# Optimization experiments

Hardware: AMD Instinct MI355X
Metric: run time of the kernel (lower is better)

The kernel has to match this reference:

```python
import jax, jax.numpy as jnp
import numpy as np

N = 16        # state dim n
M = 8         # control dim m
T = 50        # time_steps
DT = 0.01     # delta_t
SQRT_DT = DT ** 0.5
GAMMA = 0.1
SIGMA = 0.2
TAU = 0.5
H = 10        # hidden width of subnets
BATCH = 32768


def _mlp(params, x):
    W1, b1, W2, b2, W3, b3 = params
    h = jnp.tanh(x @ W1 + b1)
    h = jnp.tanh(h @ W2 + b2)
    return h @ W3 + b3


def setup_inputs() -> dict:
    key = jax.random.key(0)
    ks = jax.random.split(key, 32)

    def dense(k, i, o):
        return (jax.random.normal(k, (i, o), jnp.float32) / np.float32(np.sqrt(i)))

    inp = {
        'dw': jax.random.normal(ks[0], (T, BATCH, 1), jnp.float32) * SQRT_DT,
        'X0': jax.random.uniform(ks[1], (BATCH, N), jnp.float32),
        'A': dense(ks[2], N, N),
        'Bmat': dense(ks[3], N, M),
        'Cmat': dense(ks[4], N, N),
        'Dmat': dense(ks[5], N, M),
        # phi: (n+1) -> 10 -> 10 -> m
        'phi_W1': dense(ks[6], N + 1, H), 'phi_b1': jnp.zeros((H,), jnp.float32),
        'phi_W2': dense(ks[7], H, H),     'phi_b2': jnp.zeros((H,), jnp.float32),
        'phi_W3': dense(ks[8], H, M),     'phi_b3': jnp.zeros((M,), jnp.float32),
        # Z: (n+1) -> 10 -> 10 -> n
        'Z_W1': dense(ks[9], N + 1, H),   'Z_b1': jnp.zeros((H,), jnp.float32),
        'Z_W2': dense(ks[10], H, H),      'Z_b2': jnp.zeros((H,), jnp.float32),
        'Z_W3': dense(ks[11], H, N),      'Z_b3': jnp.zeros((N,), jnp.float32),
        # Y0: n -> 10 -> 10 -> n
        'Y0_W1': dense(ks[12], N, H),     'Y0_b1': jnp.zeros((H,), jnp.float32),
        'Y0_W2': dense(ks[13], H, H),     'Y0_b2': jnp.zeros((H,), jnp.float32),
        'Y0_W3': dense(ks[14], H, N),     'Y0_b3': jnp.zeros((N,), jnp.float32),
    }
    return inp


def reference(dw, X0, A, Bmat, Cmat, Dmat,
              phi_W1, phi_b1, phi_W2, phi_b2, phi_W3, phi_b3,
              Z_W1, Z_b1, Z_W2, Z_b2, Z_W3, Z_b3,
              Y0_W1, Y0_b1, Y0_W2, Y0_b2, Y0_W3, Y0_b3):
    phi_p = (phi_W1, phi_b1, phi_W2, phi_b2, phi_W3, phi_b3)
    Z_p = (Z_W1, Z_b1, Z_W2, Z_b2, Z_W3, Z_b3)
    Y0_p = (Y0_W1, Y0_b1, Y0_W2, Y0_b2, Y0_W3, Y0_b3)

    B = X0.shape[0]
    Y = _mlp(Y0_p, X0)                              # [B, n]
    t_grid = jnp.arange(T, dtype=X0.dtype) * DT     # [T]
    w_trap = jnp.ones((T,), X0.dtype).at[1:-1].set(2.0)  # trapezoid weights

    def step(carry, xs):
        X, Yc, lc = carry
        dwi, t, w = xs                              # dwi: [B,1]
        state = jnp.concatenate(
            [jnp.broadcast_to(t, (B, 1)).astype(X.dtype), X], axis=1)  # [B, n+1]
        Zv = _mlp(Z_p, state)                       # [B, n]
        u = _mlp(phi_p, state)                      # [B, m] (project = identity)
        # b_mult(M, x) == x @ M.T
        drift_X = X @ A.T + u @ Bmat.T + GAMMA      # [B, n]
        diffusion_X = X @ Cmat.T + u @ Dmat.T + SIGMA
        drift_Y = -(Yc @ A + Zv @ Cmat + X)         # f_x(X,u) = X
        # stop_recording branch: gradient of dH / pre_phi
        dH = Yc @ Bmat + Zv @ Dmat + u              # f_u(X,u) = u -> [B, m]
        pre_phi = jax.lax.stop_gradient(u - TAU * dH)
        Xn = X + drift_X * DT + dwi * diffusion_X
        Yn = Yc + drift_Y * DT + dwi * Zv
        lc = lc + 0.5 * DT * w * jnp.sum(jnp.square(u - pre_phi), axis=1)
        return (Xn, Yn, lc), None

    init = (X0, Y, jnp.zeros((B,), X0.dtype))
    (X, Y, loss_control), _ = jax.lax.scan(step, init, (dw, t_grid, w_trap))
    loss_bsde = jnp.sum(jnp.square(Y - X), axis=1)  # g_x(X) = X
    return jnp.stack([jnp.mean(loss_bsde), jnp.mean(loss_control)])
```

## Files before the change

kernel.cpp:

```cpp
#include <hip/hip_runtime.h>

namespace {

typedef float v4f __attribute__((ext_vector_type(4)));
typedef _Float16 half8 __attribute__((ext_vector_type(8)));
typedef unsigned int uint32;

constexpr int   kB     = 32768;
constexpr int   kT     = 50;
constexpr float kDT    = 0.01f;
constexpr float kGamma = 0.1f;
constexpr float kSigma = 0.2f;
constexpr float kTau   = 0.5f;

constexpr int kWsDwords = 13 * 256;

__device__ __forceinline__ float ftanh(float x) {
  float e = exp2f(x * 2.8853900817779268f);
  return 1.0f - 2.0f * __builtin_amdgcn_rcpf(e + 1.0f);
}

__device__ __forceinline__ uint32 pk2(float a, float b) {
  union { _Float16 h[2]; uint32 u; } z;
  z.h[0] = (_Float16)a; z.h[1] = (_Float16)b;
  return z.u;
}

__device__ __forceinline__ v4f tanh4(v4f a) {
  v4f r;
  r[0] = ftanh(a[0]); r[1] = ftanh(a[1]);
  r[2] = ftanh(a[2]); r[3] = ftanh(a[3]);
  return r;
}

#define WAVE_FENCE() asm volatile("" ::: "memory")

__global__ __launch_bounds__(256) void prep_kernel(
    const float* __restrict__ A,   const float* __restrict__ Bm,
    const float* __restrict__ Cm,  const float* __restrict__ Dm,
    const float* __restrict__ pW1, const float* __restrict__ pb1,
    const float* __restrict__ pW2, const float* __restrict__ pb2,
    const float* __restrict__ pW3, const float* __restrict__ pb3,
    const float* __restrict__ zW1, const float* __restrict__ zb1,
    const float* __restrict__ zW2, const float* __restrict__ zb2,
    const float* __restrict__ zW3, const float* __restrict__ zb3,
    const float* __restrict__ yW1, const float* __restrict__ yb1,
    const float* __restrict__ yW2, const float* __restrict__ yb2,
    const float* __restrict__ yW3, const float* __restrict__ yb3,
    uint32* __restrict__ ws, float* __restrict__ out)
{
  const int tid = threadIdx.x;
  if (tid < 2) out[tid] = 0.0f;

  auto wval = [&](int p, int m, int k) -> float {
    switch (p) {
      case 0:
        if (m >= 10) return 0.f;
        if (k == 1) return yb1[m];
        if (k >= 2 && k < 18) return yW1[(k - 2) * 10 + m];
        return 0.f;
      case 1:
        if (m >= 10) return 0.f;
        if (k < 10) return yW2[k * 10 + m];
        if (k == 10) return yb2[m];
        return 0.f;
      case 2:
        if (k < 10) return yW3[k * 16 + m];
        if (k == 10) return yb3[m];
        return 0.f;
      case 3:
        if (m >= 10) return 0.f;
        if (k == 0) return zW1[m];
        if (k == 1) return zb1[m];
        if (k < 18) return zW1[(k - 1) * 10 + m];
        return 0.f;
      case 4:
        if (m >= 10) return 0.f;
        if (k == 0) return pW1[m];
        if (k == 1) return pb1[m];
        if (k < 18) return pW1[(k - 1) * 10 + m];
        return 0.f;
      case 5:
        if (m >= 10) return 0.f;
        if (k < 10) return zW2[k * 10 + m];
        if (k == 10) return zb2[m];
        return 0.f;
      case 6:
        if (m >= 10) return 0.f;
        if (k < 10) return pW2[k * 10 + m];
        if (k == 10) return pb2[m];
        return 0.f;
      case 7:
        if (k < 10) return zW3[k * 16 + m];
        if (k == 10) return zb3[m];
        return 0.f;
      case 8:
        if (m >= 8) return 0.f;
        if (k < 10) return pW3[k * 8 + m];
        if (k == 10) return pb3[m];
        return 0.f;
      case 9:
        if (k < 16) return A[m * 16 + k];
        if (k < 24) return Bm[m * 8 + (k - 16)];
        if (k == 24) return kGamma;
        return 0.f;
      case 10:
        if (k < 16) return Cm[m * 16 + k];
        if (k < 24) return Dm[m * 8 + (k - 16)];
        if (k == 24) return kSigma;
        return 0.f;
      case 11:
        if (k < 16) return A[k * 16 + m];
        return Cm[(k - 16) * 16 + m];
      case 12:
        if (m >= 8) return 0.f;
        if (k < 16) return Bm[k * 8 + m];
        return Dm[(k - 16) * 8 + m];
    }
    return 0.f;
  };

  for (int idx = tid; idx < kWsDwords; idx += 256) {
    int p = idx >> 8, r = idx & 255;
    int lane = r >> 2, dwi = r & 3;
    int m = lane & 15, q = lane >> 4;
    int k0 = 8 * q + 2 * dwi;
    ws[idx] = pk2(wval(p, m, k0), wval(p, m, k0 + 1));
  }
}

__global__ __launch_bounds__(64)
__attribute__((amdgpu_waves_per_eu(2, 2)))
void bsde_kernel(const float* __restrict__ dw, const float* __restrict__ X0,
                 const uint32* __restrict__ wsu, float* __restrict__ out)
{
  __shared__ __align__(16) uint32 S[7][16][20];
  constexpr int B1 = 0, HZ = 1, HP = 2, GZ = 3, GP = 4, XU = 5, YZ = 6;

  const int lane = threadIdx.x;
  const int col  = lane & 15;
  const int quad = lane >> 4;
  const int e    = blockIdx.x * 16 + col;

  half8 af[13];
#pragma unroll
  for (int p = 0; p < 13; ++p) {
    union { uint4 u; half8 h; } z;
    z.u = *(const uint4*)(wsu + p * 256 + lane * 4);
    af[p] = z.h;
  }

  auto readB = [&](int b) -> half8 {
    union { uint4 u; half8 h; } z;
    z.u = *(const uint4*)&S[b][col][4 * quad];
    return z.h;
  };
  auto writeH = [&](int b, v4f t) {
    if (quad < 2) {
      uint2 w = {pk2(t[0], t[1]), pk2(t[2], t[3])};
      *(uint2*)&S[b][col][2 * quad] = w;
    } else if (quad == 2) {
      uint2 w = {pk2(t[0], t[1]), pk2(1.f, 0.f)};
      *(uint2*)&S[b][col][4] = w;
    }
  };

  for (int i = lane; i < 7 * 16 * 20; i += 64) (&S[0][0][0])[i] = 0u;
  WAVE_FENCE();

  v4f x4 = *(const v4f*)&X0[e * 16 + 4 * quad];
  {
    uint32 p01 = pk2(x4[0], x4[1]), p23 = pk2(x4[2], x4[3]);
    S[B1][col][1 + 2 * quad] = p01;
    S[B1][col][2 + 2 * quad] = p23;
    uint2 w = {p01, p23};
    *(uint2*)&S[XU][col][2 * quad] = w;
    if (lane < 16) {
      S[B1][col][0]  = pk2(0.f, 1.f);
      S[XU][col][12] = pk2(1.f, 0.f);
    }
  }
  WAVE_FENCE();

  const v4f zero4 = {0.f, 0.f, 0.f, 0.f};

  v4f y4;
  {
    v4f d = __builtin_amdgcn_mfma_f32_16x16x32_f16(af[0], readB(B1), zero4, 0, 0, 0);
    writeH(HZ, tanh4(d));
    WAVE_FENCE();
    d = __builtin_amdgcn_mfma_f32_16x16x32_f16(af[1], readB(HZ), zero4, 0, 0, 0);
    writeH(GZ, tanh4(d));
    WAVE_FENCE();
    y4 = __builtin_amdgcn_mfma_f32_16x16x32_f16(af[2], readB(GZ), zero4, 0, 0, 0);
    uint2 w = {pk2(y4[0], y4[1]), pk2(y4[2], y4[3])};
    *(uint2*)&S[YZ][col][2 * quad] = w;
  }
  WAVE_FENCE();

  float lcp = 0.0f;
  float dwv = dw[e];

#pragma unroll 1
  for (int t = 0; t < kT; ++t) {
    float dwn = (t < kT - 1) ? dw[(t + 1) * kB + e] : 0.0f;
    const float tv = (float)t * kDT;
    const float wt = (t == 0 || t == kT - 1) ? 1.0f : 2.0f;

    if (lane < 16) S[B1][col][0] = pk2(tv, 1.f);
    WAVE_FENCE();

    half8 bs = readB(B1);
    v4f hz = __builtin_amdgcn_mfma_f32_16x16x32_f16(af[3], bs, zero4, 0, 0, 0);
    v4f hp = __builtin_amdgcn_mfma_f32_16x16x32_f16(af[4], bs, zero4, 0, 0, 0);
    writeH(HZ, tanh4(hz));
    writeH(HP, tanh4(hp));
    WAVE_FENCE();

    v4f gz = __builtin_amdgcn_mfma_f32_16x16x32_f16(af[5], readB(HZ), zero4, 0, 0, 0);
    v4f gp = __builtin_amdgcn_mfma_f32_16x16x32_f16(af[6], readB(HP), zero4, 0, 0, 0);
    writeH(GZ, tanh4(gz));
    writeH(GP, tanh4(gp));
    WAVE_FENCE();

    v4f zv = __builtin_amdgcn_mfma_f32_16x16x32_f16(af[7], readB(GZ), zero4, 0, 0, 0);
    v4f uu = __builtin_amdgcn_mfma_f32_16x16x32_f16(af[8], readB(GP), zero4, 0, 0, 0);
    {
      uint2 wz = {pk2(zv[0], zv[1]), pk2(zv[2], zv[3])};
      *(uint2*)&S[YZ][col][8 + 2 * quad] = wz;
      if (quad < 2) {
        uint2 wu = {pk2(uu[0], uu[1]), pk2(uu[2], uu[3])};
        *(uint2*)&S[XU][col][8 + 2 * quad] = wu;
      }
    }
    WAVE_FENCE();

    half8 bxu = readB(XU);
    half8 byz = readB(YZ);
    v4f dx = __builtin_amdgcn_mfma_f32_16x16x32_f16(af[9],  bxu, zero4, 0, 0, 0);
    v4f fx = __builtin_amdgcn_mfma_f32_16x16x32_f16(af[10], bxu, zero4, 0, 0, 0);
    v4f dy = __builtin_amdgcn_mfma_f32_16x16x32_f16(af[11], byz, zero4, 0, 0, 0);
    v4f dh = __builtin_amdgcn_mfma_f32_16x16x32_f16(af[12], byz, zero4, 0, 0, 0);

    float ss = 0.0f;
    v4f Xn, Yn;
#pragma unroll
    for (int r = 0; r < 4; ++r) {
      Xn[r] = x4[r] + kDT * dx[r] + dwv * fx[r];
      Yn[r] = y4[r] - kDT * (dy[r] + x4[r]) + dwv * zv[r];
      float d = dh[r] + uu[r];
      ss += d * d;
    }
    lcp += (0.5f * kDT * kTau * kTau) * wt * ss;
    x4 = Xn; y4 = Yn;

    {
      uint32 p01 = pk2(x4[0], x4[1]), p23 = pk2(x4[2], x4[3]);
      S[B1][col][1 + 2 * quad] = p01;
      S[B1][col][2 + 2 * quad] = p23;
      uint2 wx = {p01, p23};
      *(uint2*)&S[XU][col][2 * quad] = wx;
      uint2 wy = {pk2(y4[0], y4[1]), pk2(y4[2], y4[3])};
      *(uint2*)&S[YZ][col][2 * quad] = wy;
    }
    dwv = dwn;
    WAVE_FENCE();
  }

  float bp = 0.0f;
#pragma unroll
  for (int r = 0; r < 4; ++r) { float d = y4[r] - x4[r]; bp += d * d; }

#pragma unroll
  for (int s = 32; s > 0; s >>= 1) {
    bp  += __shfl_down(bp,  s, 64);
    lcp += __shfl_down(lcp, s, 64);
  }
  if (lane == 0) {
    atomicAdd(&out[0], bp  * (1.0f / (float)kB));
    atomicAdd(&out[1], lcp * (1.0f / (float)kB));
  }
}

}

extern "C" void kernel_launch(void* const* d_in, const int* in_sizes, int n_in,
                              void* d_out, int out_size, void* d_ws, size_t ws_size,
                              hipStream_t stream) {
  (void)in_sizes; (void)n_in; (void)ws_size; (void)out_size;

  const float* dw  = (const float*)d_in[0];
  const float* X0  = (const float*)d_in[1];
  const float* A   = (const float*)d_in[2];
  const float* Bm  = (const float*)d_in[3];
  const float* Cm  = (const float*)d_in[4];
  const float* Dm  = (const float*)d_in[5];
  const float* pW1 = (const float*)d_in[6];
  const float* pb1 = (const float*)d_in[7];
  const float* pW2 = (const float*)d_in[8];
  const float* pb2 = (const float*)d_in[9];
  const float* pW3 = (const float*)d_in[10];
  const float* pb3 = (const float*)d_in[11];
  const float* zW1 = (const float*)d_in[12];
  const float* zb1 = (const float*)d_in[13];
  const float* zW2 = (const float*)d_in[14];
  const float* zb2 = (const float*)d_in[15];
  const float* zW3 = (const float*)d_in[16];
  const float* zb3 = (const float*)d_in[17];
  const float* yW1 = (const float*)d_in[18];
  const float* yb1 = (const float*)d_in[19];
  const float* yW2 = (const float*)d_in[20];
  const float* yb2 = (const float*)d_in[21];
  const float* yW3 = (const float*)d_in[22];
  const float* yb3 = (const float*)d_in[23];
  float* out = (float*)d_out;
  unsigned int* ws = (unsigned int*)d_ws;

  prep_kernel<<<1, 256, 0, stream>>>(
      A, Bm, Cm, Dm,
      pW1, pb1, pW2, pb2, pW3, pb3,
      zW1, zb1, zW2, zb2, zW3, zb3,
      yW1, yb1, yW2, yb2, yW3, yb3, ws, out);

  bsde_kernel<<<kB / 16, 64, 0, stream>>>(dw, X0, ws, out);
}
```

Measured before the change: 218.9 us.

## Replace LDS staging of MFMA operands with cross-lane shuffles

Removes the shared-memory scratch buffers used to turn MFMA output fragments into B-operand fragments, and builds each operand in registers with __shfl. The first-layer weight packing is reordered so that the state vector occupies K slots 0-15 and time and bias sit at slots 16-17. The aim is to cut LDS write/read round trips and the wait latency on the serial per-step dependency chain. In exchange it adds many ds_bpermute shuffles and select instructions per step, which also go through the LDS hardware.

Result: no change. 216.8 us (-0.9%).

```diff
diff --git a/kernel.cpp b/kernel.cpp
--- a/kernel.cpp
+++ b/kernel.cpp
@@ -33,7 +33,7 @@
   return r;
 }
 
-#define WAVE_FENCE() asm volatile("" ::: "memory")
+union U8 { uint32 u[4]; half8 h; };
 
 __global__ __launch_bounds__(256) void prep_kernel(
     const float* __restrict__ A,   const float* __restrict__ Bm,
@@ -56,8 +56,8 @@
     switch (p) {
       case 0:
         if (m >= 10) return 0.f;
-        if (k == 1) return yb1[m];
-        if (k >= 2 && k < 18) return yW1[(k - 2) * 10 + m];
+        if (k < 16) return yW1[k * 10 + m];
+        if (k == 17) return yb1[m];
         return 0.f;
       case 1:
         if (m >= 10) return 0.f;
@@ -70,15 +70,15 @@
         return 0.f;
       case 3:
         if (m >= 10) return 0.f;
-        if (k == 0) return zW1[m];
-        if (k == 1) return zb1[m];
-        if (k < 18) return zW1[(k - 1) * 10 + m];
+        if (k < 16) return zW1[(k + 1) * 10 + m];
+        if (k == 16) return zW1[m];
+        if (k == 17) return zb1[m];
         return 0.f;
       case 4:
         if (m >= 10) return 0.f;
-        if (k == 0) return pW1[m];
-        if (k == 1) return pb1[m];
-        if (k < 18) return pW1[(k - 1) * 10 + m];
+        if (k < 16) return pW1[(k + 1) * 10 + m];
+        if (k == 16) return pW1[m];
+        if (k == 17) return pb1[m];
         return 0.f;
       case 5:
         if (m >= 10) return 0.f;
@@ -134,9 +134,6 @@
 void bsde_kernel(const float* __restrict__ dw, const float* __restrict__ X0,
                  const uint32* __restrict__ wsu, float* __restrict__ out)
 {
-  __shared__ __align__(16) uint32 S[7][16][20];
-  constexpr int B1 = 0, HZ = 1, HP = 2, GZ = 3, GP = 4, XU = 5, YZ = 6;
-
   const int lane = threadIdx.x;
   const int col  = lane & 15;
   const int quad = lane >> 4;
@@ -150,53 +147,47 @@
     af[p] = z.h;
   }
 
-  auto readB = [&](int b) -> half8 {
-    union { uint4 u; half8 h; } z;
-    z.u = *(const uint4*)&S[b][col][4 * quad];
-    return z.h;
+  const int srcA = col + ((quad & 1) << 5);
+  const int srcH = col + ((quad == 1) ? 32 : 0);
+  const uint32 pkONE = pk2(1.f, 0.f);
+  const v4f zero4 = {0.f, 0.f, 0.f, 0.f};
+
+  auto shf = [](uint32 v, int s) -> uint32 {
+    return (uint32)__shfl((int)v, s, 64);
   };
-  auto writeH = [&](int b, v4f t) {
-    if (quad < 2) {
-      uint2 w = {pk2(t[0], t[1]), pk2(t[2], t[3])};
-      *(uint2*)&S[b][col][2 * quad] = w;
-    } else if (quad == 2) {
-      uint2 w = {pk2(t[0], t[1]), pk2(1.f, 0.f)};
-      *(uint2*)&S[b][col][4] = w;
-    }
+
+  auto buildH = [&](v4f th) -> half8 {
+    uint32 p0 = pk2(th[0], th[1]), p1 = pk2(th[2], th[3]);
+    uint32 d0 = shf(p0, srcH);
+    uint32 d1 = shf(p1, srcH);
+    uint32 d2 = shf(p0, col + 16);
+    uint32 d3 = shf(p1, col + 16);
+    U8 f;
+    f.u[0] = (quad < 2)  ? d0 : 0u;
+    f.u[1] = (quad == 0) ? d1 : ((quad == 1) ? pkONE : 0u);
+    f.u[2] = (quad == 0) ? d2 : 0u;
+    f.u[3] = (quad == 0) ? d3 : 0u;
+    return f.h;
   };
 
-  for (int i = lane; i < 7 * 16 * 20; i += 64) (&S[0][0][0])[i] = 0u;
-  WAVE_FENCE();
-
   v4f x4 = *(const v4f*)&X0[e * 16 + 4 * quad];
-  {
-    uint32 p01 = pk2(x4[0], x4[1]), p23 = pk2(x4[2], x4[3]);
-    S[B1][col][1 + 2 * quad] = p01;
-    S[B1][col][2 + 2 * quad] = p23;
-    uint2 w = {p01, p23};
-    *(uint2*)&S[XU][col][2 * quad] = w;
-    if (lane < 16) {
-      S[B1][col][0]  = pk2(0.f, 1.f);
-      S[XU][col][12] = pk2(1.f, 0.f);
-    }
-  }
-  WAVE_FENCE();
-
-  const v4f zero4 = {0.f, 0.f, 0.f, 0.f};
-
   v4f y4;
   {
-    v4f d = __builtin_amdgcn_mfma_f32_16x16x32_f16(af[0], readB(B1), zero4, 0, 0, 0);
-    writeH(HZ, tanh4(d));
-    WAVE_FENCE();
-    d = __builtin_amdgcn_mfma_f32_16x16x32_f16(af[1], readB(HZ), zero4, 0, 0, 0);
-    writeH(GZ, tanh4(d));
-    WAVE_FENCE();
-    y4 = __builtin_amdgcn_mfma_f32_16x16x32_f16(af[2], readB(GZ), zero4, 0, 0, 0);
-    uint2 w = {pk2(y4[0], y4[1]), pk2(y4[2], y4[3])};
-    *(uint2*)&S[YZ][col][2 * quad] = w;
-  }
-  WAVE_FENCE();
+    uint32 xp0 = pk2(x4[0], x4[1]), xp1 = pk2(x4[2], x4[3]);
+    uint32 XD0 = shf(xp0, srcA),      XD1 = shf(xp1, srcA);
+    uint32 XD2 = shf(xp0, srcA + 16), XD3 = shf(xp1, srcA + 16);
+    uint32 pkT = pk2(0.f, 1.f);
+    U8 b1;
+    b1.u[0] = (quad < 2) ? XD0 : ((quad == 2) ? pkT : 0u);
+    b1.u[1] = (quad < 2) ? XD1 : 0u;
+    b1.u[2] = (quad < 2) ? XD2 : 0u;
+    b1.u[3] = (quad < 2) ? XD3 : 0u;
+    v4f h = __builtin_amdgcn_mfma_f32_16x16x32_f16(af[0], b1.h, zero4, 0, 0, 0);
+    half8 hf = buildH(tanh4(h));
+    v4f g = __builtin_amdgcn_mfma_f32_16x16x32_f16(af[1], hf, zero4, 0, 0, 0);
+    half8 gf = buildH(tanh4(g));
+    y4 = __builtin_amdgcn_mfma_f32_16x16x32_f16(af[2], gf, zero4, 0, 0, 0);
+  }
 
   float lcp = 0.0f;
   float dwv = dw[e];
@@ -207,40 +198,54 @@
     const float tv = (float)t * kDT;
     const float wt = (t == 0 || t == kT - 1) ? 1.0f : 2.0f;
 
-    if (lane < 16) S[B1][col][0] = pk2(tv, 1.f);
-    WAVE_FENCE();
-
-    half8 bs = readB(B1);
-    v4f hz = __builtin_amdgcn_mfma_f32_16x16x32_f16(af[3], bs, zero4, 0, 0, 0);
-    v4f hp = __builtin_amdgcn_mfma_f32_16x16x32_f16(af[4], bs, zero4, 0, 0, 0);
-    writeH(HZ, tanh4(hz));
-    writeH(HP, tanh4(hp));
-    WAVE_FENCE();
-
-    v4f gz = __builtin_amdgcn_mfma_f32_16x16x32_f16(af[5], readB(HZ), zero4, 0, 0, 0);
-    v4f gp = __builtin_amdgcn_mfma_f32_16x16x32_f16(af[6], readB(HP), zero4, 0, 0, 0);
-    writeH(GZ, tanh4(gz));
-    writeH(GP, tanh4(gp));
-    WAVE_FENCE();
-
-    v4f zv = __builtin_amdgcn_mfma_f32_16x16x32_f16(af[7], readB(GZ), zero4, 0, 0, 0);
-    v4f uu = __builtin_amdgcn_mfma_f32_16x16x32_f16(af[8], readB(GP), zero4, 0, 0, 0);
-    {
-      uint2 wz = {pk2(zv[0], zv[1]), pk2(zv[2], zv[3])};
-      *(uint2*)&S[YZ][col][8 + 2 * quad] = wz;
-      if (quad < 2) {
-        uint2 wu = {pk2(uu[0], uu[1]), pk2(uu[2], uu[3])};
-        *(uint2*)&S[XU][col][8 + 2 * quad] = wu;
-      }
-    }
-    WAVE_FENCE();
-
-    half8 bxu = readB(XU);
-    half8 byz = readB(YZ);
-    v4f dx = __builtin_amdgcn_mfma_f32_16x16x32_f16(af[9],  bxu, zero4, 0, 0, 0);
-    v4f fx = __builtin_amdgcn_mfma_f32_16x16x32_f16(af[10], bxu, zero4, 0, 0, 0);
-    v4f dy = __builtin_amdgcn_mfma_f32_16x16x32_f16(af[11], byz, zero4, 0, 0, 0);
-    v4f dh = __builtin_amdgcn_mfma_f32_16x16x32_f16(af[12], byz, zero4, 0, 0, 0);
+    uint32 xp0 = pk2(x4[0], x4[1]), xp1 = pk2(x4[2], x4[3]);
+    uint32 yp0 = pk2(y4[0], y4[1]), yp1 = pk2(y4[2], y4[3]);
+    uint32 XD0 = shf(xp0, srcA),      XD1 = shf(xp1, srcA);
+    uint32 XD2 = shf(xp0, srcA + 16), XD3 = shf(xp1, srcA + 16);
+    uint32 YD0 = shf(yp0, srcA),      YD1 = shf(yp1, srcA);
+    uint32 YD2 = shf(yp0, srcA + 16), YD3 = shf(yp1, srcA + 16);
+
+    uint32 pkT = pk2(tv, 1.f);
+    U8 b1;
+    b1.u[0] = (quad < 2) ? XD0 : ((quad == 2) ? pkT : 0u);
+    b1.u[1] = (quad < 2) ? XD1 : 0u;
+    b1.u[2] = (quad < 2) ? XD2 : 0u;
+    b1.u[3] = (quad < 2) ? XD3 : 0u;
+
+    v4f hz = __builtin_amdgcn_mfma_f32_16x16x32_f16(af[3], b1.h, zero4, 0, 0, 0);
+    v4f hp = __builtin_amdgcn_mfma_f32_16x16x32_f16(af[4], b1.h, zero4, 0, 0, 0);
+    half8 hzf = buildH(tanh4(hz));
+    half8 hpf = buildH(tanh4(hp));
+
+    v4f gz = __builtin_amdgcn_mfma_f32_16x16x32_f16(af[5], hzf, zero4, 0, 0, 0);
+    v4f gp = __builtin_amdgcn_mfma_f32_16x16x32_f16(af[6], hpf, zero4, 0, 0, 0);
+    half8 gzf = buildH(tanh4(gz));
+    half8 gpf = buildH(tanh4(gp));
+
+    v4f zv = __builtin_amdgcn_mfma_f32_16x16x32_f16(af[7], gzf, zero4, 0, 0, 0);
+    v4f uu = __builtin_amdgcn_mfma_f32_16x16x32_f16(af[8], gpf, zero4, 0, 0, 0);
+
+    uint32 up0 = pk2(uu[0], uu[1]), up1 = pk2(uu[2], uu[3]);
+    uint32 zp0 = pk2(zv[0], zv[1]), zp1 = pk2(zv[2], zv[3]);
+    uint32 UD0 = shf(up0, col),      UD1 = shf(up1, col);
+    uint32 UD2 = shf(up0, col + 16), UD3 = shf(up1, col + 16);
+    uint32 ZD0 = shf(zp0, srcA),      ZD1 = shf(zp1, srcA);
+    uint32 ZD2 = shf(zp0, srcA + 16), ZD3 = shf(zp1, srcA + 16);
+
+    U8 xu, yz;
+    xu.u[0] = (quad < 2) ? XD0 : ((quad == 2) ? UD0 : pkONE);
+    xu.u[1] = (quad < 2) ? XD1 : ((quad == 2) ? UD1 : 0u);
+    xu.u[2] = (quad < 2) ? XD2 : ((quad == 2) ? UD2 : 0u);
+    xu.u[3] = (quad < 2) ? XD3 : ((quad == 2) ? UD3 : 0u);
+    yz.u[0] = (quad < 2) ? YD0 : ZD0;
+    yz.u[1] = (quad < 2) ? YD1 : ZD1;
+    yz.u[2] = (quad < 2) ? YD2 : ZD2;
+    yz.u[3] = (quad < 2) ? YD3 : ZD3;
+
+    v4f dx = __builtin_amdgcn_mfma_f32_16x16x32_f16(af[9],  xu.h, zero4, 0, 0, 0);
+    v4f fx = __builtin_amdgcn_mfma_f32_16x16x32_f16(af[10], xu.h, zero4, 0, 0, 0);
+    v4f dy = __builtin_amdgcn_mfma_f32_16x16x32_f16(af[11], yz.h, zero4, 0, 0, 0);
+    v4f dh = __builtin_amdgcn_mfma_f32_16x16x32_f16(af[12], yz.h, zero4, 0, 0, 0);
 
     float ss = 0.0f;
     v4f Xn, Yn;
@@ -253,18 +258,7 @@
     }
     lcp += (0.5f * kDT * kTau * kTau) * wt * ss;
     x4 = Xn; y4 = Yn;
-
-    {
-      uint32 p01 = pk2(x4[0], x4[1]), p23 = pk2(x4[2], x4[3]);
-      S[B1][col][1 + 2 * quad] = p01;
-      S[B1][col][2 + 2 * quad] = p23;
-      uint2 wx = {p01, p23};
-      *(uint2*)&S[XU][col][2 * quad] = wx;
-      uint2 wy = {pk2(y4[0], y4[1]), pk2(y4[2], y4[3])};
-      *(uint2*)&S[YZ][col][2 * quad] = wy;
-    }
     dwv = dwn;
-    WAVE_FENCE();
   }
 
   float bp = 0.0f;
```
